# Performance work log

Measured on AMD Instinct MI355X. Metric: run time of the kernel, lower is better.

The kernel has to match this reference:

```python
import jax, jax.numpy as jnp
import numpy as np

N = 50000       # nodes
E = 800000      # edges (avg degree 16)
IN_DIM = 64
H = 64          # hidden_dim
OUT_DIM = 64
R = 8           # n_relations
L = 3           # n_layers
LN_EPS = 1e-5
NEG_SLOPE = 0.2


def _layer_norm(x, g, b):
    mu = jnp.mean(x, axis=-1, keepdims=True)
    var = jnp.mean((x - mu) ** 2, axis=-1, keepdims=True)
    return (x - mu) * jax.lax.rsqrt(var + LN_EPS) * g + b


def setup_inputs() -> dict:
    key = jax.random.key(0)
    ks = jax.random.split(key, 10)
    s = 0.05
    return {
        "x": jax.random.normal(ks[0], (N, IN_DIM), jnp.float32),
        "edge_index": jax.random.randint(ks[1], (2, E), 0, N),
        "edge_type": jax.random.randint(ks[2], (E,), 0, R),
        "W_in": jax.random.normal(ks[3], (H, IN_DIM), jnp.float32) * s,
        "b_in": jnp.zeros((H,), jnp.float32),
        "W_rel": jax.random.normal(ks[4], (R, H, H), jnp.float32) * s,   # no bias
        "W_gate": jax.random.normal(ks[5], (R, H, H), jnp.float32) * s,
        "b_gate": jnp.zeros((R, H), jnp.float32),
        "W_att": jax.random.normal(ks[6], (R, 2 * H), jnp.float32) * s,  # Linear(2H,1) per relation
        "b_att": jnp.zeros((R,), jnp.float32),
        "ln_gamma": jnp.ones((L, H), jnp.float32),
        "ln_beta": jnp.zeros((L, H), jnp.float32),
        "W_out": jax.random.normal(ks[7], (OUT_DIM, H), jnp.float32) * s,
        "b_out": jnp.zeros((OUT_DIM,), jnp.float32),
    }


def reference(x, edge_index, edge_type, W_in, b_in, W_rel, W_gate, b_gate,
              W_att, b_att, ln_gamma, ln_beta, W_out, b_out):
    src, dst = edge_index[0], edge_index[1]
    Wa_src, Wa_dst = W_att[:, :H], W_att[:, H:]      # [R,H] each
    seg = dst * R + edge_type                        # combined (node, relation) scatter key
    eidx = jnp.arange(E)

    h = jax.nn.relu(x @ W_in.T + b_in)               # [N,H]

    for layer in range(L):
        h_src = h[src]                               # [E,H] gather
        h_dst = h[dst]                               # [E,H] gather
        # attention score of each edge under its own relation's Linear(2H,1)
        scores_all = h_src @ Wa_src.T + h_dst @ Wa_dst.T + b_att   # [E,R]
        scores = scores_all[eidx, edge_type]                        # [E]
        scores = jax.nn.leaky_relu(scores, NEG_SLOPE)
        # softmax over dim=0 within each relation's edge set (as in the torch code)
        m = jax.ops.segment_max(scores, edge_type, num_segments=R)
        ex = jnp.exp(scores - m[edge_type])
        denom = jax.ops.segment_sum(ex, edge_type, num_segments=R)
        att = ex / denom[edge_type]                                 # [E]
        # relation-specific linear of source features (linear commutes with gather)
        hWr = jnp.einsum('nh,rkh->nrk', h, W_rel)                   # [N,R,H]
        msg = hWr[src, edge_type] * att[:, None]                    # [E,H]
        # per-relation scatter-add into destinations
        agg = jax.ops.segment_sum(msg, seg, num_segments=N * R)     # [N*R,H]
        agg = agg.reshape(N, R, H)
        gate = jax.nn.sigmoid(jnp.einsum('nh,rkh->nrk', h, W_gate) + b_gate)  # [N,R,H]
        h_new = jnp.mean(gate * agg, axis=1)         # sum(messages)/n_relations
        h = jax.nn.relu(_layer_norm(h + h_new, ln_gamma[layer], ln_beta[layer]))

    return h @ W_out.T + b_out
```

## Files before the change

kernel.cpp:

```cpp
#include <hip/hip_runtime.h>
#include <math.h>

#define NN 50000
#define EE 800000
#define HH 64
#define RR 8
#define LL 3
#define NR (NN * RR)
#define NB ((NR + 255) / 256)
#define LN_EPS 1e-5f
#define NEG_SLOPE 0.2f
#define LDH 68
#define OTB (16 * LDH)
#define DSPREAD 64
#define NPB 80
#define NGRP 5

typedef __attribute__((ext_vector_type(8))) short bf8;
typedef __attribute__((ext_vector_type(4))) float f4;
typedef __attribute__((ext_vector_type(2))) float f2;
typedef __attribute__((ext_vector_type(8))) unsigned short us8;
typedef __attribute__((ext_vector_type(2))) unsigned int u2;
typedef __attribute__((ext_vector_type(4))) unsigned int u4;

#define WLOADP(d0, d1, sbase, vbyte) \
    asm volatile("global_load_dwordx4 %0, %2, %3 offset:0\n\t" \
                 "global_load_dwordx4 %1, %2, %3 offset:64" \
        : "=&v"(d0), "=&v"(d1) : "v"(vbyte), "s"(sbase) : "memory")

__device__ __forceinline__ unsigned short bf16r(float f) {
    unsigned u = __float_as_uint(f);
    unsigned r = u + 0x7fffu + ((u >> 16) & 1u);
    return (unsigned short)(r >> 16);
}
__device__ __forceinline__ float bf2f(unsigned short u) {
    return __uint_as_float(((unsigned)u) << 16);
}
__device__ __forceinline__ bf8 asbf8(u4 v) {
    union { u4 a; bf8 b; } c; c.a = v; return c.b;
}
__device__ __forceinline__ void stage16(const void* g, void* l) {
    __builtin_amdgcn_global_load_lds(
        (const __attribute__((address_space(1))) void*)g,
        (__attribute__((address_space(3))) void*)l, 16, 0, 0);
}

__global__ __launch_bounds__(256) void proj_in(
    const float* __restrict__ x, const float* __restrict__ W,
    const float* __restrict__ bias, const unsigned short* __restrict__ WaB,
    float* __restrict__ h, unsigned short* __restrict__ hbf,
    float* __restrict__ s_src, float* __restrict__ s_dst) {
    __shared__ float WT[64 * LDH];
    __shared__ float xs[16 * LDH];
    __shared__ float hs[16 * LDH];
    int tid = threadIdx.x;
    int n0 = blockIdx.x * 16;
    #pragma unroll
    for (int s = 0; s < 16; ++s) {
        int idx = tid + 256 * s;
        int k = idx >> 6, i = idx & 63;
        WT[i * LDH + k] = W[idx];
    }
    int row = tid >> 4, cg = tid & 15;
    {
        f4 v = ((const f4*)x)[(size_t)(n0 + row) * 16 + cg];
        *(f4*)&xs[row * LDH + cg * 4] = v;
    }
    __syncthreads();
    f4 acc;
    {
        f4 b = *(const f4*)(bias + cg * 4);
        acc = b;
        #pragma unroll
        for (int i = 0; i < 64; ++i) {
            float xv = xs[row * LDH + i];
            f4 wt = *(const f4*)&WT[i * LDH + cg * 4];
            acc[0] += xv * wt[0];
            acc[1] += xv * wt[1];
            acc[2] += xv * wt[2];
            acc[3] += xv * wt[3];
        }
        #pragma unroll
        for (int j = 0; j < 4; ++j) acc[j] = fmaxf(acc[j], 0.f);
        int n = n0 + row;
        *(f4*)(h + (size_t)n * 64 + cg * 4) = acc;
        u2 u;
        u[0] = (unsigned)bf16r(acc[0]) | ((unsigned)bf16r(acc[1]) << 16);
        u[1] = (unsigned)bf16r(acc[2]) | ((unsigned)bf16r(acc[3]) << 16);
        *(u2*)(hbf + (size_t)n * 64 + cg * 4) = u;
        *(f4*)&hs[row * LDH + cg * 4] = acc;
    }
    __syncthreads();
    if (tid < 64) {
        int lane = tid;
        int quad = lane >> 4, lr = lane & 15;
        f4 sc = (f4){0.f, 0.f, 0.f, 0.f};
        #pragma unroll
        for (int kb = 0; kb < 2; ++kb) {
            const float* p = &hs[lr * LDH + kb * 32 + quad * 8];
            bf8 a;
            #pragma unroll
            for (int j = 0; j < 8; ++j) a[j] = (short)bf16r(p[j]);
            const bf8* bw = (const bf8*)(WaB + lr * 64 + kb * 32 + quad * 8);
            sc = __builtin_amdgcn_mfma_f32_16x16x32_bf16(a, *bw, sc, 0, 0, 0);
        }
        #pragma unroll
        for (int j = 0; j < 4; ++j) {
            int n = n0 + quad * 4 + j;
            if (lr < 8) s_src[n * 8 + lr] = sc[j];
            else        s_dst[n * 8 + (lr - 8)] = sc[j];
        }
    }
}

__global__ void edge_count(const int* __restrict__ ei, const int* __restrict__ et,
                           int* __restrict__ counts, int* __restrict__ rank) {
    int e = blockIdx.x * 256 + threadIdx.x;
    int d = ei[EE + e], t = et[e];
    rank[e] = atomicAdd(&counts[d * 8 + t], 1);
}

__global__ void scan1(const int* __restrict__ counts, int* __restrict__ offs,
                      int* __restrict__ bsum) {
    __shared__ int s[256];
    int tid = threadIdx.x;
    int i = blockIdx.x * 256 + tid;
    int v = (i < NR) ? counts[i] : 0;
    s[tid] = v; __syncthreads();
    for (int d = 1; d < 256; d <<= 1) {
        int x = (tid >= d) ? s[tid - d] : 0;
        __syncthreads();
        s[tid] += x;
        __syncthreads();
    }
    if (i < NR) offs[i] = s[tid] - v;
    if (tid == 255) bsum[blockIdx.x] = s[255];
}

__global__ void scan2(int* __restrict__ bsum) {
    __shared__ int s[1024];
    int tid = threadIdx.x;
    int carry = 0;
    for (int c0 = 0; c0 < NB; c0 += 1024) {
        int i = c0 + tid;
        int v = (i < NB) ? bsum[i] : 0;
        s[tid] = v; __syncthreads();
        for (int d = 1; d < 1024; d <<= 1) {
            int x = (tid >= d) ? s[tid - d] : 0;
            __syncthreads();
            s[tid] += x;
            __syncthreads();
        }
        if (i < NB) bsum[i] = carry + s[tid] - v;
        int tot = s[1023];
        __syncthreads();
        carry += tot;
    }
}

__global__ void edge_fill(const int* __restrict__ ei, const int* __restrict__ et,
                          const int* __restrict__ rank, const int* __restrict__ offs,
                          const int* __restrict__ bsum, u2* __restrict__ spack) {
    int e = blockIdx.x * 256 + threadIdx.x;
    int s = ei[e], d = ei[EE + e], t = et[e];
    int seg = d * 8 + t;
    int slot = offs[seg] + bsum[seg >> 8] + rank[e];
    spack[slot] = (u2){(unsigned)s, (unsigned)seg};
}

__global__ void cvt_w(const float* __restrict__ Wr, const float* __restrict__ Wg,
                      const float* __restrict__ Wa, const float* __restrict__ Wo,
                      unsigned short* __restrict__ WrB, unsigned short* __restrict__ WgB,
                      unsigned short* __restrict__ WaB, unsigned short* __restrict__ WoB) {
    int i = blockIdx.x * 256 + threadIdx.x;
    WrB[i] = bf16r(Wr[i]);
    WgB[i] = bf16r(Wg[i]);
    if (i < 1024) {
        int row = i >> 6, k = i & 63;
        float v = (row < 8) ? Wa[row * 128 + k] : Wa[(row - 8) * 128 + 64 + k];
        WaB[i] = bf16r(v);
    }
    if (i < 4096) WoB[i] = bf16r(Wo[i]);
}

__global__ void denom_reduce(const float* __restrict__ dpartL,
                             float* __restrict__ idn8L) {
    __shared__ float sb[256];
    int t = threadIdx.x;
    int rb = t >> 3, ty = t & 7;
    float v = dpartL[rb * 16 + ty] + dpartL[(rb + 32) * 16 + ty];
    sb[t] = v; __syncthreads();
    for (int st = 128; st >= 8; st >>= 1) {
        if (t < st) sb[t] += sb[t + st];
        __syncthreads();
    }
    if (t < 8) idn8L[t] = 1.f / sb[t];
}

__global__ __launch_bounds__(256, 4) void gather_seg(
    const int* __restrict__ offs, const int* __restrict__ bsum,
    const u2* __restrict__ spack, const float* __restrict__ s_src,
    const float* __restrict__ s_dst, const float* __restrict__ b_att,
    const unsigned short* __restrict__ hbf_in,
    unsigned short* __restrict__ psG, float* __restrict__ dpart) {
    int tid = threadIdx.x;
    int segl = tid >> 1, half = tid & 1;
    int sidx = blockIdx.x * 128 + segl;
    int lo = offs[sidx] + bsum[sidx >> 8];
    int nxt = sidx + 1;
    int hi = (nxt < NR) ? (offs[nxt] + bsum[nxt >> 8]) : EE;
    int r = segl & 7, gn = segl >> 3;

    float bconst = s_dst[sidx] + b_att[r];

    f2 acc[16];
    #pragma unroll
    for (int i = 0; i < 16; ++i) acc[i] = (f2){0.f, 0.f};
    float exsum = 0.f;

    for (int s = lo; s < hi; s += 4) {
        int i1 = (s + 1 < hi) ? s + 1 : s;
        int i2 = (s + 2 < hi) ? s + 2 : s;
        int i3 = (s + 3 < hi) ? s + 3 : s;
        u2 sp0 = spack[s], sp1 = spack[i1], sp2 = spack[i2], sp3 = spack[i3];
        int sr0 = (int)sp0[0], sr1 = (int)sp1[0];
        int sr2 = (int)sp2[0], sr3 = (int)sp3[0];
        float sc0 = s_src[sr0 * 8 + r] + bconst;
        float sc1 = s_src[sr1 * 8 + r] + bconst;
        float sc2 = s_src[sr2 * 8 + r] + bconst;
        float sc3 = s_src[sr3 * 8 + r] + bconst;
        sc0 = (sc0 >= 0.f) ? sc0 : NEG_SLOPE * sc0;
        sc1 = (sc1 >= 0.f) ? sc1 : NEG_SLOPE * sc1;
        sc2 = (sc2 >= 0.f) ? sc2 : NEG_SLOPE * sc2;
        sc3 = (sc3 >= 0.f) ? sc3 : NEG_SLOPE * sc3;
        float a0 = __expf(sc0);
        float a1 = (s + 1 < hi) ? __expf(sc1) : 0.f;
        float a2 = (s + 2 < hi) ? __expf(sc2) : 0.f;
        float a3 = (s + 3 < hi) ? __expf(sc3) : 0.f;
        exsum += a0 + a1 + a2 + a3;
        const u4* hp0 = (const u4*)(hbf_in + ((size_t)sr0 << 6) + half * 32);
        const u4* hp1 = (const u4*)(hbf_in + ((size_t)sr1 << 6) + half * 32);
        const u4* hp2 = (const u4*)(hbf_in + ((size_t)sr2 << 6) + half * 32);
        const u4* hp3 = (const u4*)(hbf_in + ((size_t)sr3 << 6) + half * 32);
        #pragma unroll
        for (int q = 0; q < 4; ++q) {
            u4 v0 = hp0[q], v1 = hp1[q], v2 = hp2[q], v3 = hp3[q];
            #pragma unroll
            for (int k = 0; k < 4; ++k) {
                f2 w0, w1, w2, w3;
                w0[0] = __uint_as_float(v0[k] << 16);
                w0[1] = __uint_as_float(v0[k] & 0xffff0000u);
                w1[0] = __uint_as_float(v1[k] << 16);
                w1[1] = __uint_as_float(v1[k] & 0xffff0000u);
                w2[0] = __uint_as_float(v2[k] << 16);
                w2[1] = __uint_as_float(v2[k] & 0xffff0000u);
                w3[0] = __uint_as_float(v3[k] << 16);
                w3[1] = __uint_as_float(v3[k] & 0xffff0000u);
                acc[q * 4 + k] += (f2){a0, a0} * w0;
                acc[q * 4 + k] += (f2){a1, a1} * w1;
                acc[q * 4 + k] += (f2){a2, a2} * w2;
                acc[q * 4 + k] += (f2){a3, a3} * w3;
            }
        }
    }

    {
        float v = half ? 0.f : exsum;
        v += __shfl_xor(v, 1, 64);
        v += __shfl_xor(v, 16, 64);
        v += __shfl_xor(v, 32, 64);
        int lane = tid & 63;
        if ((lane & 1) == 0 && lane < 16)
            atomicAdd(&dpart[(blockIdx.x & (DSPREAD - 1)) * 16 + ((lane >> 1) & 7)], v);
    }

    unsigned short* base = psG + ((size_t)blockIdx.x << 13) + gn * 512 + r * 64;
    #pragma unroll
    for (int q = 0; q < 4; ++q) {
        us8 o;
        #pragma unroll
        for (int k = 0; k < 4; ++k) {
            o[2 * k]     = bf16r(acc[q * 4 + k][0]);
            o[2 * k + 1] = bf16r(acc[q * 4 + k][1]);
        }
        int c2 = (half * 4 + q) ^ (gn & 7);
        *(us8*)(base + c2 * 8) = o;
    }
}

#define STAGE_GRP(b, g) do { \
    int n0s_ = nb0 + (g) * 16; \
    const char* ps_src_ = (const char*)psG + (size_t)n0s_ * 1024; \
    _Pragma("unroll") \
    for (int i_ = 0; i_ < 4; ++i_) { \
        unsigned off_ = i_ * 4096 + w * 1024; \
        stage16(ps_src_ + off_ + lane * 16, (char*)psL[b] + off_); \
    } \
    unsigned a_ = (unsigned)(w * 1024 + lane * 16); \
    unsigned sa_ = a_ ^ (((a_ >> 8) & 7u) << 4); \
    stage16((const char*)(hbuf + (size_t)n0s_ * 64) + sa_, (char*)hsL[b] + a_); \
} while (0)

template<bool EMIT, bool OUT>
__global__ __launch_bounds__(256, 2) void combine_dense(
    const float* __restrict__ hbuf, const unsigned short* __restrict__ psG,
    const float* __restrict__ idn8L,
    const unsigned short* __restrict__ WrB, const unsigned short* __restrict__ WgB,
    const unsigned short* __restrict__ WaB, const unsigned short* __restrict__ WoB,
    const float* __restrict__ b_gate, const float* __restrict__ gamma,
    const float* __restrict__ beta, float* __restrict__ hout,
    unsigned short* __restrict__ hbf_out, float* __restrict__ ssrc_out,
    float* __restrict__ sdst_out, float* __restrict__ outp,
    const float* __restrict__ b_out) {
    __shared__ unsigned short psL[2][8192];
    __shared__ float hsL[2][1024];
    int tid = threadIdx.x;
    int nb0 = blockIdx.x * NPB;
    int w = tid >> 6, lane = tid & 63;
    int quad = lane >> 4, lr = lane & 15;
    int tn = w;

    STAGE_GRP(0, 0);

    unsigned rowb = (unsigned)((tn * 16 + lr) * 128 + quad * 16);
    u4 wr[8][2], wg[8][2];
    #pragma unroll
    for (int r = 0; r < 8; ++r) {
        WLOADP(wr[r][0], wr[r][1], WrB, rowb + (unsigned)r * 8192u);
        WLOADP(wg[r][0], wg[r][1], WgB, rowb + (unsigned)r * 8192u);
    }
    float bgv[8];
    #pragma unroll
    for (int r = 0; r < 8; ++r) bgv[r] = b_gate[r * 64 + tn * 16 + lr];
    f4 gmv = *(const f4*)(gamma + (tid & 15) * 4);
    f4 btv = *(const f4*)(beta + (tid & 15) * 4);
    f4 id0 = *(const f4*)idn8L;
    f4 id1 = *(const f4*)(idn8L + 4);
    float idnv[8] = {id0[0], id0[1], id0[2], id0[3],
                     id1[0], id1[1], id1[2], id1[3]};

    for (int g = 0; g < NGRP; ++g) {
        int cb = g & 1;
        int n0 = nb0 + g * 16;
        if (g + 1 < NGRP) {
            STAGE_GRP(cb ^ 1, g + 1);
            asm volatile("s_waitcnt vmcnt(5)" ::: "memory");
        } else {
            asm volatile("s_waitcnt vmcnt(0)" ::: "memory");
        }
        __builtin_amdgcn_sched_barrier(0);
        __builtin_amdgcn_s_barrier();

        bf8 a_h[2];
        #pragma unroll
        for (int kb = 0; kb < 2; ++kb) {
            unsigned c0 = (unsigned)(kb * 8 + quad * 2)     ^ (unsigned)(lr & 7);
            unsigned c1 = (unsigned)(kb * 8 + quad * 2 + 1) ^ (unsigned)(lr & 7);
            f4 p0 = *(const f4*)((const char*)hsL[cb] + lr * 256 + c0 * 16);
            f4 p1 = *(const f4*)((const char*)hsL[cb] + lr * 256 + c1 * 16);
            bf8 a;
            #pragma unroll
            for (int j = 0; j < 4; ++j) a[j] = (short)bf16r(p0[j]);
            #pragma unroll
            for (int j = 0; j < 4; ++j) a[4 + j] = (short)bf16r(p1[j]);
            a_h[kb] = a;
        }

        f4 acc = (f4){0.f, 0.f, 0.f, 0.f};
        #pragma unroll
        for (int r = 0; r < 8; ++r) {
            bf8 a_p[2];
            #pragma unroll
            for (int kb = 0; kb < 2; ++kb) {
                unsigned c = (unsigned)(kb * 4 + quad) ^ (unsigned)(lr & 7);
                a_p[kb] = *(const bf8*)((const char*)psL[cb] + lr * 1024 + r * 128 + c * 16);
            }
            f4 aggc = (f4){0.f, 0.f, 0.f, 0.f};
            f4 gacc = (f4){0.f, 0.f, 0.f, 0.f};
            aggc = __builtin_amdgcn_mfma_f32_16x16x32_bf16(a_p[0], asbf8(wr[r][0]), aggc, 0, 0, 0);
            gacc = __builtin_amdgcn_mfma_f32_16x16x32_bf16(a_h[0], asbf8(wg[r][0]), gacc, 0, 0, 0);
            aggc = __builtin_amdgcn_mfma_f32_16x16x32_bf16(a_p[1], asbf8(wr[r][1]), aggc, 0, 0, 0);
            gacc = __builtin_amdgcn_mfma_f32_16x16x32_bf16(a_h[1], asbf8(wg[r][1]), gacc, 0, 0, 0);
            #pragma unroll
            for (int j = 0; j < 4; ++j) {
                float gt = 1.f / (1.f + __expf(-(gacc[j] + bgv[r])));
                acc[j] += gt * (aggc[j] * idnv[r]);
            }
        }
        __syncthreads();

        float* ps_f = (float*)psL[cb];
        #pragma unroll
        for (int j = 0; j < 4; ++j) {
            int row = quad * 4 + j;
            int col = tn * 16 + lr;
            unsigned y = (unsigned)(row * 256 + col * 4);
            float hres = *(const float*)((const char*)hsL[cb] + (y ^ (((unsigned)(row & 7)) << 4)));
            ps_f[row * LDH + col] = hres + acc[j] * 0.125f;
        }
        __syncthreads();

        {
            int row = tid >> 4, c = tid & 15;
            int n = n0 + row;
            f4 tv = *(const f4*)&ps_f[row * LDH + c * 4];
            float s1 = tv[0] + tv[1] + tv[2] + tv[3];
            float s2 = tv[0]*tv[0] + tv[1]*tv[1] + tv[2]*tv[2] + tv[3]*tv[3];
            #pragma unroll
            for (int off = 1; off <= 8; off <<= 1) {
                s1 += __shfl_xor(s1, off, 64);
                s2 += __shfl_xor(s2, off, 64);
            }
            float mu = s1 * (1.f / 64.f);
            float var = s2 * (1.f / 64.f) - mu * mu;
            float rs = rsqrtf(var + LN_EPS);
            f4 ov;
            #pragma unroll
            for (int j = 0; j < 4; ++j)
                ov[j] = fmaxf((tv[j] - mu) * rs * gmv[j] + btv[j], 0.f);
            if (!OUT)
                *(f4*)(hout + (size_t)n * 64 + c * 4) = ov;
            *(f4*)&ps_f[OTB + row * LDH + c * 4] = ov;
            if (EMIT) {
                u2 u;
                u[0] = (unsigned)bf16r(ov[0]) | ((unsigned)bf16r(ov[1]) << 16);
                u[1] = (unsigned)bf16r(ov[2]) | ((unsigned)bf16r(ov[3]) << 16);
                *(u2*)(hbf_out + (size_t)n * 64 + c * 4) = u;
            }
        }

        if (EMIT) {
            __syncthreads();
            if (w == 0) {
                f4 sc = (f4){0.f, 0.f, 0.f, 0.f};
                #pragma unroll
                for (int kb = 0; kb < 2; ++kb) {
                    const float* p = &ps_f[OTB + lr * LDH + kb * 32 + quad * 8];
                    bf8 a;
                    #pragma unroll
                    for (int j = 0; j < 8; ++j) a[j] = (short)bf16r(p[j]);
                    const bf8* bw = (const bf8*)(WaB + lr * 64 + kb * 32 + quad * 8);
                    sc = __builtin_amdgcn_mfma_f32_16x16x32_bf16(a, *bw, sc, 0, 0, 0);
                }
                #pragma unroll
                for (int j = 0; j < 4; ++j) {
                    int n = n0 + quad * 4 + j;
                    if (lr < 8) ssrc_out[n * 8 + lr] = sc[j];
                    else        sdst_out[n * 8 + (lr - 8)] = sc[j];
                }
            }
        }

        if (OUT) {
            __syncthreads();
            f4 oc = (f4){0.f, 0.f, 0.f, 0.f};
            #pragma unroll
            for (int kb = 0; kb < 2; ++kb) {
                const float* p = &ps_f[OTB + lr * LDH + kb * 32 + quad * 8];
                bf8 a;
                #pragma unroll
                for (int j = 0; j < 8; ++j) a[j] = (short)bf16r(p[j]);
                const bf8* bw = (const bf8*)(WoB + ((tn * 16 + lr) * 64 + kb * 32 + quad * 8));
                oc = __builtin_amdgcn_mfma_f32_16x16x32_bf16(a, *bw, oc, 0, 0, 0);
            }
            float bo = b_out[tn * 16 + lr];
            #pragma unroll
            for (int j = 0; j < 4; ++j)
                outp[(size_t)(n0 + quad * 4 + j) * 64 + tn * 16 + lr] = oc[j] + bo;
        }
        __syncthreads();
    }
}

extern "C" void kernel_launch(void* const* d_in, const int* in_sizes, int n_in,
                              void* d_out, int out_size, void* d_ws, size_t ws_size,
                              hipStream_t stream) {
    const float* x      = (const float*)d_in[0];
    const int*   ei     = (const int*)d_in[1];
    const int*   et     = (const int*)d_in[2];
    const float* W_in   = (const float*)d_in[3];
    const float* b_in   = (const float*)d_in[4];
    const float* W_rel  = (const float*)d_in[5];
    const float* W_gate = (const float*)d_in[6];
    const float* b_gate = (const float*)d_in[7];
    const float* W_att  = (const float*)d_in[8];
    const float* b_att  = (const float*)d_in[9];
    const float* ln_g   = (const float*)d_in[10];
    const float* ln_b   = (const float*)d_in[11];
    const float* W_out  = (const float*)d_in[12];
    const float* b_out  = (const float*)d_in[13];
    float* out = (float*)d_out;

    float* h0 = (float*)d_out;

    char* ws = (char*)d_ws;
    float* h1 = (float*)ws;                     ws += (size_t)NN * 64 * 4;
    unsigned short* hbfA = (unsigned short*)ws; ws += (size_t)NN * 64 * 2;
    unsigned short* hbfB = (unsigned short*)ws; ws += (size_t)NN * 64 * 2;
    float* s_src = (float*)ws;                  ws += (size_t)NN * 8 * 4;
    float* s_dst = (float*)ws;                  ws += (size_t)NN * 8 * 4;
    unsigned short* WrB = (unsigned short*)ws;  ws += (size_t)RR * 64 * 64 * 2;
    unsigned short* WgB = (unsigned short*)ws;  ws += (size_t)RR * 64 * 64 * 2;
    unsigned short* WaB = (unsigned short*)ws;  ws += 2048;
    unsigned short* WoB = (unsigned short*)ws;  ws += 8192;
    int* counts = (int*)ws;                     ws += (size_t)NR * 4;
    float* dpart = (float*)ws;                  ws += 3 * DSPREAD * 16 * 4;
    float* idn8G = (float*)ws;                  ws += 3 * 16 * 4;
    int* offs = (int*)ws;                       ws += (size_t)NR * 4;
    int* bsum = (int*)ws;                       ws += 6400;
    int* rank = (int*)ws;                       ws += (size_t)EE * 4;
    u2* spack = (u2*)ws;                        ws += (size_t)EE * 8;
    unsigned short* psG = (unsigned short*)ws;  ws += (size_t)NR * 64 * 2;

    hipMemsetAsync(counts, 0, (size_t)NR * 4 + 3 * DSPREAD * 16 * 4, stream);
    cvt_w<<<128, 256, 0, stream>>>(W_rel, W_gate, W_att, W_out, WrB, WgB, WaB, WoB);
    edge_count<<<EE / 256, 256, 0, stream>>>(ei, et, counts, rank);
    scan1<<<NB, 256, 0, stream>>>(counts, offs, bsum);
    scan2<<<1, 1024, 0, stream>>>(bsum);
    edge_fill<<<EE / 256, 256, 0, stream>>>(ei, et, rank, offs, bsum, spack);
    proj_in<<<NN / 16, 256, 0, stream>>>(x, W_in, b_in, WaB, h0, hbfA, s_src, s_dst);

    const int tiles16 = NN / 16;
    const int tiles80 = NN / NPB;
    float* hA = h0;  float* hB = h1;
    unsigned short* bfA = hbfA;  unsigned short* bfB = hbfB;
    for (int layer = 0; layer < LL; ++layer) {
        float* dpl = dpart + (size_t)layer * DSPREAD * 16;
        float* idn = idn8G + (size_t)layer * 16;
        gather_seg<<<tiles16, 256, 0, stream>>>(offs, bsum, spack, s_src, s_dst,
                                                b_att, bfA, psG, dpl);
        denom_reduce<<<1, 256, 0, stream>>>(dpl, idn);
        if (layer < LL - 1) {
            combine_dense<true, false><<<tiles80, 256, 0, stream>>>(
                hA, psG, idn, WrB, WgB, WaB, WoB, b_gate,
                ln_g + layer * 64, ln_b + layer * 64,
                hB, bfB, s_src, s_dst, out, b_out);
        } else {
            combine_dense<false, true><<<tiles80, 256, 0, stream>>>(
                hA, psG, idn, WrB, WgB, WaB, WoB, b_gate,
                ln_g + layer * 64, ln_b + layer * 64,
                hB, bfB, s_src, s_dst, out, b_out);
        }
        float* tf = hA; hA = hB; hB = tf;
        unsigned short* tb = bfA; bfA = bfB; bfB = tb;
    }
}
```

Before: 412.8 us.

## Fuse edge gather-aggregation into combine kernel and split softmax denominator pass

```diff
diff --git a/kernel.cpp b/kernel.cpp
--- a/kernel.cpp
+++ b/kernel.cpp
@@ -183,6 +183,31 @@
     if (i < 4096) WoB[i] = bf16r(Wo[i]);
 }
 
+__global__ void denom_pass(const u2* __restrict__ spack,
+                           const float* __restrict__ s_src,
+                           const float* __restrict__ s_dst,
+                           const float* __restrict__ b_att,
+                           float* __restrict__ dpart) {
+    __shared__ float lsum[4][8];
+    int tid = threadIdx.x;
+    if (tid < 32) lsum[tid >> 3][tid & 7] = 0.f;
+    __syncthreads();
+    int slot = blockIdx.x * 256 + tid;
+    u2 sp = spack[slot];
+    int src = (int)sp[0];
+    int seg = (int)sp[1];
+    int t = seg & 7;
+    float sc = s_src[src * 8 + t] + s_dst[seg] + b_att[t];
+    sc = (sc >= 0.f) ? sc : NEG_SLOPE * sc;
+    float ex = __expf(sc);
+    atomicAdd(&lsum[tid >> 6][t], ex);
+    __syncthreads();
+    if (tid < 8) {
+        float v = lsum[0][tid] + lsum[1][tid] + lsum[2][tid] + lsum[3][tid];
+        atomicAdd(&dpart[(blockIdx.x & (DSPREAD - 1)) * 16 + tid], v);
+    }
+}
+
 __global__ void denom_reduce(const float* __restrict__ dpartL,
                              float* __restrict__ idn8L) {
     __shared__ float sb[256];
@@ -197,84 +222,53 @@
     if (t < 8) idn8L[t] = 1.f / sb[t];
 }
 
-__global__ __launch_bounds__(256, 4) void gather_seg(
+__device__ __forceinline__ void gather_group(
+    int sidx0, int segl, int half,
     const int* __restrict__ offs, const int* __restrict__ bsum,
     const u2* __restrict__ spack, const float* __restrict__ s_src,
-    const float* __restrict__ s_dst, const float* __restrict__ b_att,
+    const float* __restrict__ s_dst, float bav,
     const unsigned short* __restrict__ hbf_in,
-    unsigned short* __restrict__ psG, float* __restrict__ dpart) {
-    int tid = threadIdx.x;
-    int segl = tid >> 1, half = tid & 1;
-    int sidx = blockIdx.x * 128 + segl;
+    unsigned short* psb) {
+    int sidx = sidx0 + segl;
     int lo = offs[sidx] + bsum[sidx >> 8];
     int nxt = sidx + 1;
     int hi = (nxt < NR) ? (offs[nxt] + bsum[nxt >> 8]) : EE;
     int r = segl & 7, gn = segl >> 3;
-
-    float bconst = s_dst[sidx] + b_att[r];
+    float bconst = s_dst[sidx] + bav;
 
     f2 acc[16];
     #pragma unroll
     for (int i = 0; i < 16; ++i) acc[i] = (f2){0.f, 0.f};
-    float exsum = 0.f;
-
-    for (int s = lo; s < hi; s += 4) {
+
+    for (int s = lo; s < hi; s += 2) {
         int i1 = (s + 1 < hi) ? s + 1 : s;
-        int i2 = (s + 2 < hi) ? s + 2 : s;
-        int i3 = (s + 3 < hi) ? s + 3 : s;
-        u2 sp0 = spack[s], sp1 = spack[i1], sp2 = spack[i2], sp3 = spack[i3];
+        u2 sp0 = spack[s], sp1 = spack[i1];
         int sr0 = (int)sp0[0], sr1 = (int)sp1[0];
-        int sr2 = (int)sp2[0], sr3 = (int)sp3[0];
         float sc0 = s_src[sr0 * 8 + r] + bconst;
         float sc1 = s_src[sr1 * 8 + r] + bconst;
-        float sc2 = s_src[sr2 * 8 + r] + bconst;
-        float sc3 = s_src[sr3 * 8 + r] + bconst;
         sc0 = (sc0 >= 0.f) ? sc0 : NEG_SLOPE * sc0;
         sc1 = (sc1 >= 0.f) ? sc1 : NEG_SLOPE * sc1;
-        sc2 = (sc2 >= 0.f) ? sc2 : NEG_SLOPE * sc2;
-        sc3 = (sc3 >= 0.f) ? sc3 : NEG_SLOPE * sc3;
         float a0 = __expf(sc0);
         float a1 = (s + 1 < hi) ? __expf(sc1) : 0.f;
-        float a2 = (s + 2 < hi) ? __expf(sc2) : 0.f;
-        float a3 = (s + 3 < hi) ? __expf(sc3) : 0.f;
-        exsum += a0 + a1 + a2 + a3;
         const u4* hp0 = (const u4*)(hbf_in + ((size_t)sr0 << 6) + half * 32);
         const u4* hp1 = (const u4*)(hbf_in + ((size_t)sr1 << 6) + half * 32);
-        const u4* hp2 = (const u4*)(hbf_in + ((size_t)sr2 << 6) + half * 32);
-        const u4* hp3 = (const u4*)(hbf_in + ((size_t)sr3 << 6) + half * 32);
         #pragma unroll
         for (int q = 0; q < 4; ++q) {
-            u4 v0 = hp0[q], v1 = hp1[q], v2 = hp2[q], v3 = hp3[q];
+            u4 v0 = hp0[q], v1 = hp1[q];
             #pragma unroll
             for (int k = 0; k < 4; ++k) {
-                f2 w0, w1, w2, w3;
+                f2 w0, w1;
                 w0[0] = __uint_as_float(v0[k] << 16);
                 w0[1] = __uint_as_float(v0[k] & 0xffff0000u);
                 w1[0] = __uint_as_float(v1[k] << 16);
                 w1[1] = __uint_as_float(v1[k] & 0xffff0000u);
-                w2[0] = __uint_as_float(v2[k] << 16);
-                w2[1] = __uint_as_float(v2[k] & 0xffff0000u);
-                w3[0] = __uint_as_float(v3[k] << 16);
-                w3[1] = __uint_as_float(v3[k] & 0xffff0000u);
                 acc[q * 4 + k] += (f2){a0, a0} * w0;
                 acc[q * 4 + k] += (f2){a1, a1} * w1;
-                acc[q * 4 + k] += (f2){a2, a2} * w2;
-                acc[q * 4 + k] += (f2){a3, a3} * w3;
-            }
-        }
-    }
-
-    {
-        float v = half ? 0.f : exsum;
-        v += __shfl_xor(v, 1, 64);
-        v += __shfl_xor(v, 16, 64);
-        v += __shfl_xor(v, 32, 64);
-        int lane = tid & 63;
-        if ((lane & 1) == 0 && lane < 16)
-            atomicAdd(&dpart[(blockIdx.x & (DSPREAD - 1)) * 16 + ((lane >> 1) & 7)], v);
-    }
-
-    unsigned short* base = psG + ((size_t)blockIdx.x << 13) + gn * 512 + r * 64;
+            }
+        }
+    }
+
+    unsigned short* base = psb + gn * 512 + r * 64;
     #pragma unroll
     for (int q = 0; q < 4; ++q) {
         us8 o;
@@ -288,23 +282,21 @@
     }
 }
 
-#define STAGE_GRP(b, g) do { \
+#define STAGE_HS(b, g) do { \
     int n0s_ = nb0 + (g) * 16; \
-    const char* ps_src_ = (const char*)psG + (size_t)n0s_ * 1024; \
-    _Pragma("unroll") \
-    for (int i_ = 0; i_ < 4; ++i_) { \
-        unsigned off_ = i_ * 4096 + w * 1024; \
-        stage16(ps_src_ + off_ + lane * 16, (char*)psL[b] + off_); \
-    } \
     unsigned a_ = (unsigned)(w * 1024 + lane * 16); \
     unsigned sa_ = a_ ^ (((a_ >> 8) & 7u) << 4); \
-    stage16((const char*)(hbuf + (size_t)n0s_ * 64) + sa_, (char*)hsL[b] + a_); \
+    stage16((const float*)((const char*)(hbuf + (size_t)n0s_ * 64) + sa_), \
+            (char*)hsL[b] + a_); \
 } while (0)
 
 template<bool EMIT, bool OUT>
-__global__ __launch_bounds__(256, 2) void combine_dense(
-    const float* __restrict__ hbuf, const unsigned short* __restrict__ psG,
+__global__ __launch_bounds__(256, 2) void combine_fused(
+    const float* __restrict__ hbuf, const unsigned short* __restrict__ hbf_in,
     const float* __restrict__ idn8L,
+    const int* __restrict__ offs, const int* __restrict__ bsum,
+    const u2* __restrict__ spack, const float* __restrict__ s_srcI,
+    const float* __restrict__ s_dstI, const float* __restrict__ b_att,
     const unsigned short* __restrict__ WrB, const unsigned short* __restrict__ WgB,
     const unsigned short* __restrict__ WaB, const unsigned short* __restrict__ WoB,
     const float* __restrict__ b_gate, const float* __restrict__ gamma,
@@ -312,15 +304,16 @@
     unsigned short* __restrict__ hbf_out, float* __restrict__ ssrc_out,
     float* __restrict__ sdst_out, float* __restrict__ outp,
     const float* __restrict__ b_out) {
-    __shared__ unsigned short psL[2][8192];
-    __shared__ float hsL[2][1024];
+    __shared__ alignas(16) unsigned short psL[2][8192];
+    __shared__ alignas(16) float hsL[2][1024];
     int tid = threadIdx.x;
     int nb0 = blockIdx.x * NPB;
     int w = tid >> 6, lane = tid & 63;
     int quad = lane >> 4, lr = lane & 15;
     int tn = w;
-
-    STAGE_GRP(0, 0);
+    int segl = tid >> 1, half = tid & 1;
+
+    STAGE_HS(0, 0);
 
     unsigned rowb = (unsigned)((tn * 16 + lr) * 128 + quad * 16);
     u4 wr[8][2], wg[8][2];
@@ -338,18 +331,24 @@
     f4 id1 = *(const f4*)(idn8L + 4);
     float idnv[8] = {id0[0], id0[1], id0[2], id0[3],
                      id1[0], id1[1], id1[2], id1[3]};
+    float bav = b_att[segl & 7];
+
+    asm volatile("s_waitcnt vmcnt(0)" ::: "memory");
+    __builtin_amdgcn_sched_barrier(0);
+
+    gather_group(nb0 * 8, segl, half, offs, bsum, spack, s_srcI, s_dstI,
+                 bav, hbf_in, psL[0]);
 
     for (int g = 0; g < NGRP; ++g) {
         int cb = g & 1;
         int n0 = nb0 + g * 16;
+        __syncthreads();
+
         if (g + 1 < NGRP) {
-            STAGE_GRP(cb ^ 1, g + 1);
-            asm volatile("s_waitcnt vmcnt(5)" ::: "memory");
-        } else {
-            asm volatile("s_waitcnt vmcnt(0)" ::: "memory");
-        }
-        __builtin_amdgcn_sched_barrier(0);
-        __builtin_amdgcn_s_barrier();
+            STAGE_HS(cb ^ 1, g + 1);
+            gather_group((nb0 + (g + 1) * 16) * 8, segl, half, offs, bsum,
+                         spack, s_srcI, s_dstI, bav, hbf_in, psL[cb ^ 1]);
+        }
 
         bf8 a_h[2];
         #pragma unroll
@@ -468,7 +467,6 @@
             for (int j = 0; j < 4; ++j)
                 outp[(size_t)(n0 + quad * 4 + j) * 64 + tn * 16 + lr] = oc[j] + bo;
         }
-        __syncthreads();
     }
 }
 
@@ -497,8 +495,10 @@
     float* h1 = (float*)ws;                     ws += (size_t)NN * 64 * 4;
     unsigned short* hbfA = (unsigned short*)ws; ws += (size_t)NN * 64 * 2;
     unsigned short* hbfB = (unsigned short*)ws; ws += (size_t)NN * 64 * 2;
-    float* s_src = (float*)ws;                  ws += (size_t)NN * 8 * 4;
-    float* s_dst = (float*)ws;                  ws += (size_t)NN * 8 * 4;
+    float* s_srcA = (float*)ws;                 ws += (size_t)NN * 8 * 4;
+    float* s_dstA = (float*)ws;                 ws += (size_t)NN * 8 * 4;
+    float* s_srcB = (float*)ws;                 ws += (size_t)NN * 8 * 4;
+    float* s_dstB = (float*)ws;                 ws += (size_t)NN * 8 * 4;
     unsigned short* WrB = (unsigned short*)ws;  ws += (size_t)RR * 64 * 64 * 2;
     unsigned short* WgB = (unsigned short*)ws;  ws += (size_t)RR * 64 * 64 * 2;
     unsigned short* WaB = (unsigned short*)ws;  ws += 2048;
@@ -510,7 +510,6 @@
     int* bsum = (int*)ws;                       ws += 6400;
     int* rank = (int*)ws;                       ws += (size_t)EE * 4;
     u2* spack = (u2*)ws;                        ws += (size_t)EE * 8;
-    unsigned short* psG = (unsigned short*)ws;  ws += (size_t)NR * 64 * 2;
 
     hipMemsetAsync(counts, 0, (size_t)NR * 4 + 3 * DSPREAD * 16 * 4, stream);
     cvt_w<<<128, 256, 0, stream>>>(W_rel, W_gate, W_att, W_out, WrB, WgB, WaB, WoB);
@@ -518,30 +517,34 @@
     scan1<<<NB, 256, 0, stream>>>(counts, offs, bsum);
     scan2<<<1, 1024, 0, stream>>>(bsum);
     edge_fill<<<EE / 256, 256, 0, stream>>>(ei, et, rank, offs, bsum, spack);
-    proj_in<<<NN / 16, 256, 0, stream>>>(x, W_in, b_in, WaB, h0, hbfA, s_src, s_dst);
-
-    const int tiles16 = NN / 16;
+    proj_in<<<NN / 16, 256, 0, stream>>>(x, W_in, b_in, WaB, h0, hbfA, s_srcA, s_dstA);
+
     const int tiles80 = NN / NPB;
     float* hA = h0;  float* hB = h1;
     unsigned short* bfA = hbfA;  unsigned short* bfB = hbfB;
+    float* ssI = s_srcA;  float* sdI = s_dstA;
+    float* ssO = s_srcB;  float* sdO = s_dstB;
     for (int layer = 0; layer < LL; ++layer) {
         float* dpl = dpart + (size_t)layer * DSPREAD * 16;
         float* idn = idn8G + (size_t)layer * 16;
-        gather_seg<<<tiles16, 256, 0, stream>>>(offs, bsum, spack, s_src, s_dst,
-                                                b_att, bfA, psG, dpl);
+        denom_pass<<<EE / 256, 256, 0, stream>>>(spack, ssI, sdI, b_att, dpl);
         denom_reduce<<<1, 256, 0, stream>>>(dpl, idn);
         if (layer < LL - 1) {
-            combine_dense<true, false><<<tiles80, 256, 0, stream>>>(
-                hA, psG, idn, WrB, WgB, WaB, WoB, b_gate,
+            combine_fused<true, false><<<tiles80, 256, 0, stream>>>(
+                hA, bfA, idn, offs, bsum, spack, ssI, sdI, b_att,
+                WrB, WgB, WaB, WoB, b_gate,
                 ln_g + layer * 64, ln_b + layer * 64,
-                hB, bfB, s_src, s_dst, out, b_out);
+                hB, bfB, ssO, sdO, out, b_out);
         } else {
-            combine_dense<false, true><<<tiles80, 256, 0, stream>>>(
-                hA, psG, idn, WrB, WgB, WaB, WoB, b_gate,
+            combine_fused<false, true><<<tiles80, 256, 0, stream>>>(
+                hA, bfA, idn, offs, bsum, spack, ssI, sdI, b_att,
+                WrB, WgB, WaB, WoB, b_gate,
                 ln_g + layer * 64, ln_b + layer * 64,
-                hB, bfB, s_src, s_dst, out, b_out);
+                hB, bfB, ssO, sdO, out, b_out);
         }
         float* tf = hA; hA = hB; hB = tf;
         unsigned short* tb = bfA; bfA = bfB; bfB = tb;
-    }
-}
+        float* ts = ssI; ssI = ssO; ssO = ts;
+        float* td = sdI; sdI = sdO; sdO = td;
+    }
+}
```

Measured after the change: 456.9 us. 1.11x slower.
